# Performance work log

Hardware: AMD Instinct MI355X
Metric: run time of the kernel (lower is better)

## Reference

```python
import jax, jax.numpy as jnp
import numpy as np

H_, W_, KNN, KO = 64, 64, 32, 32
TAU, ETA, LAMBDA0, ALPHA = 1.5, 8.0, 0.001, 10.0
A_, B_, BETA, BETA_P = 1.0, 0.0, 8.0, 8.0
SMOOTH_KS, SMOOTH_SIGMA, EPS = 5, 1.0, 1e-6


def _base_grid(h, w):
    ys = jnp.arange(h, dtype=jnp.float32)
    xs = jnp.arange(w, dtype=jnp.float32)
    yy, xx = jnp.meshgrid(ys, xs, indexing='ij')
    return jnp.stack([xx.reshape(-1), yy.reshape(-1)], axis=-1)  # (N,2) as (x,y)


def _offset_bins(K_o, h, w):
    maxr = (h ** 2 + w ** 2) ** 0.5 * 0.5
    ks = jnp.arange(1, K_o + 1, dtype=jnp.float32)
    angles = 2.0 * jnp.pi * (ks - 1) / K_o
    radii = 0.2 * maxr + 0.6 * maxr * (ks - 1) / (K_o - 1 + 1e-9)
    return jnp.stack([radii * jnp.cos(angles), radii * jnp.sin(angles)], axis=-1)  # (K_o,2)


def _gaussian_kernel(ks, sigma):
    ax = jnp.arange(-(ks // 2), ks // 2 + 1, dtype=jnp.float32)  # matches torch -ks//2+1 .. ks//2 for odd ks
    xx, yy = jnp.meshgrid(ax, ax, indexing='ij')
    k = jnp.exp(-(xx ** 2 + yy ** 2) / (2.0 * sigma ** 2))
    return (k / k.sum()).reshape(1, 1, ks, ks)


def setup_inputs() -> dict:
    key = jax.random.key(0)
    k1, k2 = jax.random.split(key)
    B, N = 2, H_ * W_
    E = jax.random.normal(k1, (B, N, 256), dtype=jnp.float32)
    A0 = jax.random.uniform(k2, (B, N, N), dtype=jnp.float32)
    return {
        'E': E,
        'A0': A0,
        'P': _base_grid(H_, W_),
        'bins': _offset_bins(KO, H_, W_),
        'smooth_kernel': _gaussian_kernel(SMOOTH_KS, SMOOTH_SIGMA),
    }


def reference(E, A0, P, bins, smooth_kernel):
    B, N, _ = A0.shape
    # top-k neighbors per row (sorted descending, like torch.topk)
    topk_vals, topk_idx = jax.lax.top_k(A0, KNN)  # (B,N,k)

    # offset vectors to neighbors
    p_j = P[topk_idx]                              # (B,N,k,2)
    v = p_j - P[None, :, None, :]                  # (B,N,k,2)
    diff = v[..., None, :] - bins[None, None, None, :, :]   # (B,N,k,K_o,2)
    dist2 = (diff ** 2).sum(-1)                    # (B,N,k,K_o)
    kappa = jnp.exp(-dist2 / (2.0 * TAU ** 2 + 1e-12))

    # global bin histogram and softmax weights
    Hbins = (topk_vals[..., None] * kappa).sum(axis=(1, 2))   # (B,K_o)
    Wsoft = jax.nn.softmax(ETA * Hbins, axis=-1)              # (B,K_o)

    R_edges = LAMBDA0 + (Wsoft[:, None, None, :] * kappa).sum(-1)  # (B,N,k)
    tildeA = topk_vals * R_edges
    A1_edges = tildeA / (tildeA.sum(-1, keepdims=True) + EPS)

    # entropy -> backgroundness U
    p = jax.nn.softmax(ALPHA * A1_edges, axis=-1)
    entropy = -(p * jnp.log(p + EPS)).sum(-1)      # (B,N)
    U = jax.nn.sigmoid(-A_ * entropy + B_)
    m = 1.0 - U

    # mask both endpoints of each edge
    m_j = jax.vmap(jnp.take)(m, topk_idx)          # (B,N,k)
    hatA = m[:, :, None] * A1_edges * m_j
    A2_edges = hatA / (hatA.sum(-1, keepdims=True) + EPS)

    # scatter sparse edges back to dense NxN (row indices unique per row)
    b_idx = jnp.arange(B)[:, None, None]
    n_idx = jnp.arange(N)[None, :, None]
    A2_dense = jnp.zeros((B, N, N), A2_edges.dtype).at[b_idx, n_idx, topk_idx].set(A2_edges)
    A2_dense = A2_dense / (A2_dense.sum(-1, keepdims=True) + EPS)

    # directional evidence
    exp_fwd = jnp.exp(BETA * A2_dense)
    exp_rev = jnp.swapaxes(exp_fwd, -1, -2)
    P_dir = exp_fwd / (exp_fwd + exp_rev + EPS)
    eye = jnp.eye(N, dtype=A2_dense.dtype)
    P_dir = P_dir * (1.0 - eye)                    # zero diagonal
    s_ev = (A2_dense * P_dir).sum(-1)
    A2_T = jnp.swapaxes(A2_dense, -1, -2)
    t_ev = (A2_T * (1.0 - jnp.swapaxes(P_dir, -1, -2))).sum(-1)
    pi_src = s_ev / (s_ev + t_ev + EPS)
    pi_tgt = 1.0 - pi_src

    # spatial attention map
    W_mean = Wsoft.mean(0)                         # (K_o,)
    chi = (kappa * W_mean[None, None, None, :]).sum(-1)       # (B,N,k)
    w_local = jax.nn.softmax(BETA_P * A2_edges, axis=-1)
    q = (w_local * chi).sum(-1)                    # (B,N)
    A1_map = q.reshape(B, 1, H_, W_)
    pad = SMOOTH_KS // 2
    smoothed = jax.lax.conv_general_dilated(A1_map, smooth_kernel, (1, 1), [(pad, pad), (pad, pad)])
    A1_map = jax.nn.sigmoid(smoothed)              # (B,1,h,w)

    return (A2_dense, U, pi_src, pi_tgt, A1_map)
```

## Files before the change

### kernel.cpp

```cpp
#include <hip/hip_runtime.h>
#include <math.h>

#define NN 4096
#define KK 32
#define KOb 32
#define BB 2
#define NSLOT 64

constexpr float EPS = 1e-6f;

#define WS_VALS   0
#define WS_IDX    (WS_VALS + BB*NN*KK)
#define WS_HBP    (WS_IDX + BB*NN*KK)
#define WS_A1     (WS_HBP + BB*NSLOT*KOb)
#define WS_M      (WS_A1 + BB*NN*KK)
#define WS_CHI    (WS_M + BB*NN)
#define WS_A2     (WS_CHI + BB*NN*KK)
#define WS_SEV    (WS_A2 + BB*NN*KK)
#define WS_TEV    (WS_SEV + BB*NN)
#define WS_Q      (WS_TEV + BB*NN)

#define OUT_A2   0
#define OUT_U    ((size_t)BB*NN*NN)
#define OUT_PSRC (OUT_U + BB*NN)
#define OUT_PTGT (OUT_PSRC + BB*NN)
#define OUT_MAP  (OUT_PTGT + BB*NN)

__device__ __forceinline__ unsigned int fkey(float x) {
    unsigned int u = __float_as_uint(x);
    return u ^ ((unsigned int)((int)u >> 31) | 0x80000000u);
}
__device__ __forceinline__ float key2f(unsigned int k) {
    unsigned int u = (k & 0x80000000u) ? (k ^ 0x80000000u) : ~k;
    return __uint_as_float(u);
}

__global__ __launch_bounds__(256) void k_topk(const float* __restrict__ A0,
                                              const float* __restrict__ bins,
                                              float* __restrict__ ws) {
    __shared__ unsigned long long cand[4][64];
    __shared__ float sbins[2 * KOb];
    __shared__ float shb[KOb];

    const int t = threadIdx.x;
    const int wv = t >> 6, lane = t & 63;
    const int R = blockIdx.x * 4 + wv;
    const int b = blockIdx.x >> 10;
    const int r = R & (NN - 1);

    if (t < 2 * KOb) sbins[t] = bins[t];
    if (t < KOb) shb[t] = 0.f;

    const float4* row4 = (const float4*)(A0 + (size_t)R * NN);
    unsigned int key[64];
    #pragma unroll
    for (int j4 = 0; j4 < 16; ++j4) {
        const float4 f = row4[j4 * 64 + lane];
        key[4 * j4 + 0] = fkey(f.x);
        key[4 * j4 + 1] = fkey(f.y);
        key[4 * j4 + 2] = fkey(f.z);
        key[4 * j4 + 3] = fkey(f.w);
    }

    unsigned int lo = 0u, hi = 0xFFFFFFFFu;
    int cnt = NN, myc = 64, it = 0;
    while (cnt > 64) {
        unsigned int mid;
        if (it == 0)      mid = 0xBF7E0000u;
        else if (it == 1) mid = 0xBF7C4000u;
        else              mid = lo + ((hi - lo) >> 1);
        if (mid <= lo || mid >= hi) mid = lo + ((hi - lo) >> 1);
        if (mid == lo) break;
        int cl = 0;
        #pragma unroll
        for (int j = 0; j < 64; ++j) cl += (key[j] > mid) ? 1 : 0;
        int c = cl;
        #pragma unroll
        for (int m = 32; m >= 1; m >>= 1) c += __shfl_xor(c, m);
        if (c >= KK) { lo = mid; cnt = c; myc = cl; } else hi = mid;
        if (++it > 48) break;
    }
    if (lo == 0u) {
        int cl = 0;
        #pragma unroll
        for (int j = 0; j < 64; ++j) cl += (key[j] > 0u) ? 1 : 0;
        myc = cl;
    }

    int pre = myc;
    #pragma unroll
    for (int m = 1; m < 64; m <<= 1) {
        const int o = __shfl_up(pre, m);
        if (lane >= m) pre += o;
    }
    pre -= myc;

    int slot = pre;
    #pragma unroll
    for (int j = 0; j < 64; ++j) {
        if (key[j] > lo && slot < 64) {
            const unsigned int gidx = (unsigned int)((j >> 2) * 256 + lane * 4 + (j & 3));
            cand[wv][slot] = ((unsigned long long)key[j] << 32)
                           | (unsigned long long)(4095u - gidx);
            ++slot;
        }
    }
    const int ncand = (cnt < 64) ? cnt : 64;
    __syncthreads();

    const unsigned long long cd = (lane < ncand) ? cand[wv][lane] : 0ull;
    int rank = 0;
    #pragma unroll
    for (int i = 0; i < 64; ++i) {
        const unsigned long long o = __shfl(cd, i);
        rank += (o > cd) ? 1 : 0;
    }

    const bool sel = (lane < ncand) && (rank < KK);
    float val = 0.f; int gidx = 0;
    if (sel) {
        val = key2f((unsigned int)(cd >> 32));
        gidx = 4095 - (int)(cd & 0xFFFull);
        ws[WS_VALS + (size_t)R * KK + rank] = val;
        ((int*)(ws + WS_IDX))[(size_t)R * KK + rank] = gidx;
    }

    if (sel) {
        const float dx0 = (float)((gidx & 63) - (r & 63));
        const float dy0 = (float)((gidx >> 6) - (r >> 6));
        #pragma unroll
        for (int oo = 0; oo < KOb; ++oo) {
            const int o = (oo + lane) & 31;
            const float dx = dx0 - sbins[2 * o], dy = dy0 - sbins[2 * o + 1];
            atomicAdd(&shb[o], val * __expf(-(dx * dx + dy * dy) * (1.0f / 4.5f)));
        }
    }
    __syncthreads();
    if (t < KOb)
        atomicAdd(ws + WS_HBP + b * (NSLOT * KOb) + (blockIdx.x & (NSLOT - 1)) * KOb + t,
                  shb[t]);
}

__global__ __launch_bounds__(256) void k_row1(const float* __restrict__ bins,
                                              float* __restrict__ ws,
                                              float* __restrict__ out_u) {
    __shared__ float sbins[2 * KOb], sHB[BB * KOb], swsoft[BB * KOb], swmean[KOb];
    const int t = threadIdx.x;
    if (t < 2 * KOb) sbins[t] = bins[t];
    if (t >= 64 && t < 64 + BB * KOb) sHB[t - 64] = 0.f;
    __syncthreads();

    #pragma unroll
    for (int rep = 0; rep < 2; ++rep) {
        const int task = t + 256 * rep;
        const int bo = task & 63;
        const int sg = task >> 6;
        float ps = 0.f;
        #pragma unroll
        for (int s = 0; s < 8; ++s)
            ps += ws[WS_HBP + (bo >> 5) * (NSLOT * KOb) + (sg * 8 + s) * KOb + (bo & 31)];
        atomicAdd(&sHB[bo], ps);
    }
    __syncthreads();
    if (t < BB * KOb) {
        const float h = 8.0f * sHB[t];
        float mx = h;
        #pragma unroll
        for (int m = 16; m >= 1; m >>= 1) mx = fmaxf(mx, __shfl_xor(mx, m));
        const float e = __expf(h - mx);
        float s = e;
        #pragma unroll
        for (int m = 16; m >= 1; m >>= 1) s += __shfl_xor(s, m);
        swsoft[t] = e / s;
    }
    if (t < KOb) swmean[t] = 0.5f * (swsoft[t] + swsoft[KOb + t]);
    __syncthreads();

    const int wv = t >> 6, lane = t & 63;
    const int R = blockIdx.x * 4 + wv;
    const int b = R >> 12;
    const int r = R & (NN - 1);
    const bool act = lane < 32;
    const int k = lane;

    float val = 0.f, Redge = 0.f, chi = 0.f;
    if (act) {
        val = ws[WS_VALS + (size_t)R * KK + k];
        const int c = ((int*)(ws + WS_IDX))[(size_t)R * KK + k];
        const float dx0 = (float)((c & 63) - (r & 63));
        const float dy0 = (float)((c >> 6) - (r >> 6));
        float racc = 0.f, cacc = 0.f;
        for (int o = 0; o < KOb; ++o) {
            const float dx = dx0 - sbins[2 * o], dy = dy0 - sbins[2 * o + 1];
            const float kap = __expf(-(dx * dx + dy * dy) * (1.0f / 4.5f));
            racc += swsoft[b * KOb + o] * kap;
            cacc += swmean[o] * kap;
        }
        Redge = 0.001f + racc;
        chi = cacc;
    }
    const float tilde = act ? val * Redge : 0.f;
    float s = tilde;
    #pragma unroll
    for (int m = 16; m >= 1; m >>= 1) s += __shfl_xor(s, m);
    const float a1 = tilde / (s + EPS);

    const float z = act ? 10.f * a1 : -1e30f;
    float mz = z;
    #pragma unroll
    for (int m = 16; m >= 1; m >>= 1) mz = fmaxf(mz, __shfl_xor(mz, m));
    const float e = act ? __expf(z - mz) : 0.f;
    float se = e;
    #pragma unroll
    for (int m = 16; m >= 1; m >>= 1) se += __shfl_xor(se, m);
    const float p = e / se;
    const float ent_t = act ? -p * __logf(p + EPS) : 0.f;
    float ent = ent_t;
    #pragma unroll
    for (int m = 16; m >= 1; m >>= 1) ent += __shfl_xor(ent, m);
    const float U = 1.f / (1.f + __expf(ent));

    if (act) {
        ws[WS_A1  + (size_t)R * KK + k] = a1;
        ws[WS_CHI + (size_t)R * KK + k] = chi;
    }
    if (lane == 0) { out_u[R] = U; ws[WS_M + R] = 1.f - U; }
}

__global__ __launch_bounds__(256) void k_row2d(float* __restrict__ ws,
                                               float* __restrict__ outA2) {
    __shared__ float srow[NN];
    __shared__ float sdv[KK];
    __shared__ int   sidx[KK];
    const int R = blockIdx.x;
    const int b = R >> 12;
    const int r = R & (NN - 1);
    const int t = threadIdx.x;

    const int gid = blockIdx.x * 256 + t;
    if (gid < BB * NN) ws[WS_TEV + gid] = 0.f;

    float4* s4 = (float4*)srow;
    const float4 z4 = make_float4(0.f, 0.f, 0.f, 0.f);
    #pragma unroll
    for (int i = 0; i < 4; ++i) s4[t + 256 * i] = z4;

    if (t < 64) {
        const int lane = t;
        const bool act = lane < 32;
        const int k = lane;
        const float mi = ws[WS_M + R];
        float a1 = 0.f; int c = 0; float mj = 0.f;
        if (act) {
            a1 = ws[WS_A1 + (size_t)R * KK + k];
            c = ((int*)(ws + WS_IDX))[(size_t)R * KK + k];
            mj = ws[WS_M + b * NN + c];
        }
        const float hat = act ? mi * a1 * mj : 0.f;
        float S = hat;
        #pragma unroll
        for (int m = 16; m >= 1; m >>= 1) S += __shfl_xor(S, m);
        const float a2e = hat / (S + EPS);
        float S2 = a2e;
        #pragma unroll
        for (int m = 16; m >= 1; m >>= 1) S2 += __shfl_xor(S2, m);
        const float dv = a2e / (S2 + EPS);

        const float z = act ? 8.f * a2e : -1e30f;
        float mz = z;
        #pragma unroll
        for (int m = 16; m >= 1; m >>= 1) mz = fmaxf(mz, __shfl_xor(mz, m));
        const float e = act ? __expf(z - mz) : 0.f;
        float se = e;
        #pragma unroll
        for (int m = 16; m >= 1; m >>= 1) se += __shfl_xor(se, m);
        const float wl = e / se;
        const float chi = act ? ws[WS_CHI + (size_t)R * KK + k] : 0.f;
        float q = act ? wl * chi : 0.f;
        #pragma unroll
        for (int m = 16; m >= 1; m >>= 1) q += __shfl_xor(q, m);
        if (lane == 0) ws[WS_Q + R] = q;

        if (act) {
            ws[WS_A2 + (size_t)R * KK + k] = dv;
            sdv[k] = dv;
            sidx[k] = c;
        }
    }
    __syncthreads();
    if (t < KK) srow[sidx[t]] = sdv[t];
    __syncthreads();
    float4* o4 = (float4*)(outA2 + (size_t)b * NN * NN + (size_t)r * NN);
    #pragma unroll
    for (int i = 0; i < 4; ++i) o4[t + 256 * i] = s4[t + 256 * i];
}

__global__ __launch_bounds__(256) void k_dir(float* __restrict__ ws,
                                             const float* __restrict__ A2d) {
    const int t = threadIdx.x;
    const int wv = t >> 6, lane = t & 63;
    const int R = blockIdx.x * 4 + wv;
    const int b = R >> 12;
    const int r = R & (NN - 1);
    const bool act = lane < 32;
    const int k = lane;

    float a = 0.f; int c = r;
    if (act) {
        a = ws[WS_A2 + (size_t)R * KK + k];
        c = ((int*)(ws + WS_IDX))[(size_t)R * KK + k];
    }
    float pdir = 0.f;
    if (act && c != r) {
        const float arev = A2d[(size_t)b * NN * NN + (size_t)c * NN + r];
        const float ef = __expf(8.f * a), er = __expf(8.f * arev);
        pdir = ef / (ef + er + EPS);
    }
    float s = a * pdir;
    #pragma unroll
    for (int m = 16; m >= 1; m >>= 1) s += __shfl_xor(s, m);
    if (lane == 0) ws[WS_SEV + R] = s;
    if (act) atomicAdd(ws + WS_TEV + b * NN + c, a * (1.f - pdir));
}

__global__ void k_tail(const float* __restrict__ ws, const float* __restrict__ kern,
                       float* __restrict__ out_psrc, float* __restrict__ out_ptgt,
                       float* __restrict__ out_map) {
    const int i = blockIdx.x * 256 + threadIdx.x;
    const float s = ws[WS_SEV + i], tv = ws[WS_TEV + i];
    const float ps = s / (s + tv + EPS);
    out_psrc[i] = ps;
    out_ptgt[i] = 1.f - ps;

    const int b = i >> 12;
    const int pix = i & 4095;
    const int y = pix >> 6, x = pix & 63;
    float acc = 0.f;
    #pragma unroll
    for (int ky = 0; ky < 5; ++ky) {
        const int yy = y + ky - 2;
        if (yy < 0 || yy >= 64) continue;
        #pragma unroll
        for (int kx = 0; kx < 5; ++kx) {
            const int xx = x + kx - 2;
            if (xx < 0 || xx >= 64) continue;
            acc += ws[WS_Q + b * 4096 + yy * 64 + xx] * kern[ky * 5 + kx];
        }
    }
    out_map[i] = 1.f / (1.f + __expf(-acc));
}

extern "C" void kernel_launch(void* const* d_in, const int* in_sizes, int n_in,
                              void* d_out, int out_size, void* d_ws, size_t ws_size,
                              hipStream_t stream) {
    const float* A0   = (const float*)d_in[1];
    const float* bins = (const float*)d_in[3];
    const float* kern = (const float*)d_in[4];
    float* out = (float*)d_out;
    float* ws  = (float*)d_ws;

    hipMemsetAsync(ws + WS_HBP, 0, BB * NSLOT * KOb * sizeof(float), stream);

    k_topk <<<BB * NN / 4,   256, 0, stream>>>(A0, bins, ws);
    k_row1 <<<BB * NN / 4,   256, 0, stream>>>(bins, ws, out + OUT_U);
    k_row2d<<<BB * NN,       256, 0, stream>>>(ws, out);
    k_dir  <<<BB * NN / 4,   256, 0, stream>>>(ws, out);
    k_tail <<<BB * NN / 256, 256, 0, stream>>>(ws, kern,
                                               out + OUT_PSRC, out + OUT_PTGT,
                                               out + OUT_MAP);
}
```

Baseline: 333.9 us.

## Use one block per row for top-k and sparse reverse lookup in direction pass

The top-k kernel now assigns a whole 256-thread block to each row instead of one wavefront per row. Each thread holds 16 keys rather than 64, which cuts register pressure, and the threshold search now combines counts across waves through shared memory with barriers. The histogram accumulation is spread over all threads, with shuffle reductions replacing 32 per-lane shared atomics. The direction kernel now finds the reverse edge weight by scanning the neighbor's 32 top-k indices instead of a random read from the dense 4096x4096 output, which avoids scattered global memory traffic at the cost of a short index scan.

New measurement: 296.8 us. -11.1%, faster.

```diff
diff --git a/kernel.cpp b/kernel.cpp
--- a/kernel.cpp
+++ b/kernel.cpp
@@ -38,32 +38,35 @@
 __global__ __launch_bounds__(256) void k_topk(const float* __restrict__ A0,
                                               const float* __restrict__ bins,
                                               float* __restrict__ ws) {
-    __shared__ unsigned long long cand[4][64];
     __shared__ float sbins[2 * KOb];
+    __shared__ int   scnt[4];
+    __shared__ int   swtot[4];
+    __shared__ unsigned long long cand[64];
+    __shared__ float selv[KK], seldx[KK], seldy[KK];
     __shared__ float shb[KOb];
 
     const int t = threadIdx.x;
     const int wv = t >> 6, lane = t & 63;
-    const int R = blockIdx.x * 4 + wv;
-    const int b = blockIdx.x >> 10;
+    const int R = blockIdx.x;
+    const int b = R >> 12;
     const int r = R & (NN - 1);
 
     if (t < 2 * KOb) sbins[t] = bins[t];
     if (t < KOb) shb[t] = 0.f;
 
     const float4* row4 = (const float4*)(A0 + (size_t)R * NN);
-    unsigned int key[64];
-    #pragma unroll
-    for (int j4 = 0; j4 < 16; ++j4) {
-        const float4 f = row4[j4 * 64 + lane];
-        key[4 * j4 + 0] = fkey(f.x);
-        key[4 * j4 + 1] = fkey(f.y);
-        key[4 * j4 + 2] = fkey(f.z);
-        key[4 * j4 + 3] = fkey(f.w);
+    unsigned int key[16];
+    #pragma unroll
+    for (int i = 0; i < 4; ++i) {
+        const float4 f = row4[i * 256 + t];
+        key[4 * i + 0] = fkey(f.x);
+        key[4 * i + 1] = fkey(f.y);
+        key[4 * i + 2] = fkey(f.z);
+        key[4 * i + 3] = fkey(f.w);
     }
 
     unsigned int lo = 0u, hi = 0xFFFFFFFFu;
-    int cnt = NN, myc = 64, it = 0;
+    int cnt = NN, it = 0;
     while (cnt > 64) {
         unsigned int mid;
         if (it == 0)      mid = 0xBF7E0000u;
@@ -73,71 +76,82 @@
         if (mid == lo) break;
         int cl = 0;
         #pragma unroll
-        for (int j = 0; j < 64; ++j) cl += (key[j] > mid) ? 1 : 0;
+        for (int j = 0; j < 16; ++j) cl += (key[j] > mid) ? 1 : 0;
         int c = cl;
         #pragma unroll
         for (int m = 32; m >= 1; m >>= 1) c += __shfl_xor(c, m);
-        if (c >= KK) { lo = mid; cnt = c; myc = cl; } else hi = mid;
+        if (lane == 0) scnt[wv] = c;
+        __syncthreads();
+        const int ctot = scnt[0] + scnt[1] + scnt[2] + scnt[3];
+        __syncthreads();
+        if (ctot >= KK) { lo = mid; cnt = ctot; } else hi = mid;
         if (++it > 48) break;
     }
-    if (lo == 0u) {
-        int cl = 0;
-        #pragma unroll
-        for (int j = 0; j < 64; ++j) cl += (key[j] > 0u) ? 1 : 0;
-        myc = cl;
-    }
-
-    int pre = myc;
+
+    int cl = 0;
+    #pragma unroll
+    for (int j = 0; j < 16; ++j) cl += (key[j] > lo) ? 1 : 0;
+    int inc = cl;
     #pragma unroll
     for (int m = 1; m < 64; m <<= 1) {
-        const int o = __shfl_up(pre, m);
-        if (lane >= m) pre += o;
-    }
-    pre -= myc;
-
-    int slot = pre;
-    #pragma unroll
-    for (int j = 0; j < 64; ++j) {
+        const int o = __shfl_up(inc, m);
+        if (lane >= m) inc += o;
+    }
+    if (lane == 63) swtot[wv] = inc;
+    __syncthreads();
+    int off = inc - cl;
+    #pragma unroll
+    for (int w = 0; w < 4; ++w) if (w < wv) off += swtot[w];
+    const int nc0 = swtot[0] + swtot[1] + swtot[2] + swtot[3];
+    const int ncand = (nc0 < 64) ? nc0 : 64;
+
+    int slot = off;
+    #pragma unroll
+    for (int j = 0; j < 16; ++j) {
         if (key[j] > lo && slot < 64) {
-            const unsigned int gidx = (unsigned int)((j >> 2) * 256 + lane * 4 + (j & 3));
-            cand[wv][slot] = ((unsigned long long)key[j] << 32)
-                           | (unsigned long long)(4095u - gidx);
+            const unsigned int gidx = (unsigned int)((j >> 2) * 1024 + t * 4 + (j & 3));
+            cand[slot] = ((unsigned long long)key[j] << 32)
+                       | (unsigned long long)(4095u - gidx);
             ++slot;
         }
     }
-    const int ncand = (cnt < 64) ? cnt : 64;
-    __syncthreads();
-
-    const unsigned long long cd = (lane < ncand) ? cand[wv][lane] : 0ull;
-    int rank = 0;
-    #pragma unroll
-    for (int i = 0; i < 64; ++i) {
-        const unsigned long long o = __shfl(cd, i);
-        rank += (o > cd) ? 1 : 0;
-    }
-
-    const bool sel = (lane < ncand) && (rank < KK);
-    float val = 0.f; int gidx = 0;
-    if (sel) {
-        val = key2f((unsigned int)(cd >> 32));
-        gidx = 4095 - (int)(cd & 0xFFFull);
-        ws[WS_VALS + (size_t)R * KK + rank] = val;
-        ((int*)(ws + WS_IDX))[(size_t)R * KK + rank] = gidx;
-    }
-
-    if (sel) {
-        const float dx0 = (float)((gidx & 63) - (r & 63));
-        const float dy0 = (float)((gidx >> 6) - (r >> 6));
-        #pragma unroll
-        for (int oo = 0; oo < KOb; ++oo) {
-            const int o = (oo + lane) & 31;
-            const float dx = dx0 - sbins[2 * o], dy = dy0 - sbins[2 * o + 1];
-            atomicAdd(&shb[o], val * __expf(-(dx * dx + dy * dy) * (1.0f / 4.5f)));
-        }
+    __syncthreads();
+
+    if (t < 64) {
+        const unsigned long long cd = (t < ncand) ? cand[t] : 0ull;
+        int rank = 0;
+        #pragma unroll
+        for (int i = 0; i < 64; ++i) {
+            const unsigned long long o = __shfl(cd, i);
+            rank += (o > cd) ? 1 : 0;
+        }
+        if (t < ncand && rank < KK) {
+            const float val = key2f((unsigned int)(cd >> 32));
+            const int gidx = 4095 - (int)(cd & 0xFFFull);
+            ws[WS_VALS + (size_t)R * KK + rank] = val;
+            ((int*)(ws + WS_IDX))[(size_t)R * KK + rank] = gidx;
+            selv[rank]  = val;
+            seldx[rank] = (float)((gidx & 63) - (r & 63));
+            seldy[rank] = (float)((gidx >> 6) - (r >> 6));
+        }
+    }
+    __syncthreads();
+
+    const int e = t >> 3;
+    const float v = selv[e], dx0 = seldx[e], dy0 = seldy[e];
+    #pragma unroll
+    for (int jj = 0; jj < 4; ++jj) {
+        const int o = (lane & 7) * 4 + jj;
+        const float dx = dx0 - sbins[2 * o], dy = dy0 - sbins[2 * o + 1];
+        float contrib = v * __expf(-(dx * dx + dy * dy) * (1.0f / 4.5f));
+        contrib += __shfl_xor(contrib, 8);
+        contrib += __shfl_xor(contrib, 16);
+        contrib += __shfl_xor(contrib, 32);
+        if ((lane >> 3) == 0) atomicAdd(&shb[o], contrib);
     }
     __syncthreads();
     if (t < KOb)
-        atomicAdd(ws + WS_HBP + b * (NSLOT * KOb) + (blockIdx.x & (NSLOT - 1)) * KOb + t,
+        atomicAdd(ws + WS_HBP + b * (NSLOT * KOb) + (R & (NSLOT - 1)) * KOb + t,
                   shb[t]);
 }
 
@@ -295,8 +309,7 @@
     for (int i = 0; i < 4; ++i) o4[t + 256 * i] = s4[t + 256 * i];
 }
 
-__global__ __launch_bounds__(256) void k_dir(float* __restrict__ ws,
-                                             const float* __restrict__ A2d) {
+__global__ __launch_bounds__(256) void k_dir(float* __restrict__ ws) {
     const int t = threadIdx.x;
     const int wv = t >> 6, lane = t & 63;
     const int R = blockIdx.x * 4 + wv;
@@ -312,7 +325,18 @@
     }
     float pdir = 0.f;
     if (act && c != r) {
-        const float arev = A2d[(size_t)b * NN * NN + (size_t)c * NN + r];
+        const int4* irow = (const int4*)((const int*)(ws + WS_IDX)
+                                         + (size_t)(b * NN + c) * KK);
+        int p = -1;
+        #pragma unroll
+        for (int q = 0; q < 8; ++q) {
+            const int4 i4 = irow[q];
+            if (i4.x == r) p = q * 4 + 0;
+            if (i4.y == r) p = q * 4 + 1;
+            if (i4.z == r) p = q * 4 + 2;
+            if (i4.w == r) p = q * 4 + 3;
+        }
+        const float arev = (p >= 0) ? ws[WS_A2 + (size_t)(b * NN + c) * KK + p] : 0.f;
         const float ef = __expf(8.f * a), er = __expf(8.f * arev);
         pdir = ef / (ef + er + EPS);
     }
@@ -361,10 +385,10 @@
 
     hipMemsetAsync(ws + WS_HBP, 0, BB * NSLOT * KOb * sizeof(float), stream);
 
-    k_topk <<<BB * NN / 4,   256, 0, stream>>>(A0, bins, ws);
+    k_topk <<<BB * NN,       256, 0, stream>>>(A0, bins, ws);
     k_row1 <<<BB * NN / 4,   256, 0, stream>>>(bins, ws, out + OUT_U);
     k_row2d<<<BB * NN,       256, 0, stream>>>(ws, out);
-    k_dir  <<<BB * NN / 4,   256, 0, stream>>>(ws, out);
+    k_dir  <<<BB * NN / 4,   256, 0, stream>>>(ws);
     k_tail <<<BB * NN / 256, 256, 0, stream>>>(ws, kern,
                                                out + OUT_PSRC, out + OUT_PTGT,
                                                out + OUT_MAP);
```
